# Kernel optimization log

Hardware: AMD Instinct MI355X
Metric: run time of the kernel (lower is better)

Reference implementation:

```python
import jax, jax.numpy as jnp
import numpy as np
from jax import lax

B, T, I, H = 64, 784, 1, 600


def setup_inputs() -> dict:
    key = jax.random.key(0)
    ks = jax.random.split(key, 9)
    k = 1.0 / np.sqrt(H)  # pytorch LSTMCell/Linear init scale
    x = jax.random.normal(ks[0], (B, T, I), dtype=jnp.float32)
    hs0 = jax.random.normal(ks[1], (B, H), dtype=jnp.float32)
    cs0 = jax.random.normal(ks[2], (B, H), dtype=jnp.float32)
    W_ih = jax.random.normal(ks[3], (4 * H, I), dtype=jnp.float32) * k
    W_hh = jax.random.normal(ks[4], (4 * H, H), dtype=jnp.float32) * k
    b_ih = jax.random.normal(ks[5], (4 * H,), dtype=jnp.float32) * k
    b_hh = jax.random.normal(ks[6], (4 * H,), dtype=jnp.float32) * k
    W_out = jax.random.normal(ks[7], (10, H), dtype=jnp.float32) * k
    b_out = jax.random.normal(ks[8], (10,), dtype=jnp.float32) * k
    return {"x": x, "hs0": hs0, "cs0": cs0, "W_ih": W_ih, "W_hh": W_hh,
            "b_ih": b_ih, "b_hh": b_hh, "W_out": W_out, "b_out": b_out}


def reference(x, hs0, cs0, W_ih, W_hh, b_ih, b_hh, W_out, b_out):
    # Precompute input projections for all timesteps in one GEMM: [B,T,4H]
    pre = jnp.einsum('bti,gi->btg', x, W_ih) + b_ih + b_hh
    pre_t = jnp.swapaxes(pre, 0, 1)  # [T,B,4H]

    def step(carry, p):
        h, c = carry
        gates = p + h @ W_hh.T  # [B,4H], pytorch gate order i,f,g,o
        i, f, g, o = jnp.split(gates, 4, axis=-1)
        c = jax.nn.sigmoid(f) * c + jax.nn.sigmoid(i) * jnp.tanh(g)
        h = jax.nn.sigmoid(o) * jnp.tanh(c)
        return (h, c), None

    (h, _), _ = lax.scan(step, (hs0, cs0), pre_t)
    return h @ W_out.T + b_out  # [B,10]
```

## Files before the change

### kernel.cpp

```cpp
#include <hip/hip_runtime.h>
#include <math.h>

#define BB 64
#define TT 784
#define HH 600
#define CG 50
#define SGN 4
#define CPW 12
#define BW 16
#define NWG (CG*SGN)
#define BLOCK 512
#define HB4 (BW*150)
#define LDS_BYTES (84*1024)

typedef float f2v __attribute__((ext_vector_type(2)));

__device__ __forceinline__ void ldg5_bypass(const float4* g0, const float4* g1,
                                            const float4* g2, const float4* g3,
                                            const float4* g4,
                                            float4& a, float4& b, float4& c,
                                            float4& d, float4& e) {
    asm volatile(
        "global_load_dwordx4 %0, %5, off sc0 sc1\n\t"
        "global_load_dwordx4 %1, %6, off sc0 sc1\n\t"
        "global_load_dwordx4 %2, %7, off sc0 sc1\n\t"
        "global_load_dwordx4 %3, %8, off sc0 sc1\n\t"
        "global_load_dwordx4 %4, %9, off sc0 sc1\n\t"
        "s_waitcnt vmcnt(0)"
        : "=&v"(a), "=&v"(b), "=&v"(c), "=&v"(d), "=&v"(e)
        : "v"(g0), "v"(g1), "v"(g2), "v"(g3), "v"(g4)
        : "memory");
}

__device__ __forceinline__ void ldg6_slice(const float4* base,
                                           float4& a, float4& b, float4& c,
                                           float4& d, float4& e, float4& f) {
    asm volatile(
        "global_load_dwordx4 %0, %6, off sc0 sc1\n\t"
        "global_load_dwordx4 %1, %6, off offset:16 sc0 sc1\n\t"
        "global_load_dwordx4 %2, %6, off offset:32 sc0 sc1\n\t"
        "global_load_dwordx4 %3, %6, off offset:2400 sc0 sc1\n\t"
        "global_load_dwordx4 %4, %6, off offset:2416 sc0 sc1\n\t"
        "global_load_dwordx4 %5, %6, off offset:2432 sc0 sc1\n\t"
        "s_waitcnt vmcnt(0)"
        : "=&v"(a), "=&v"(b), "=&v"(c), "=&v"(d), "=&v"(e), "=&v"(f)
        : "v"(base) : "memory");
}

__device__ __forceinline__ void stg_bypass(float* p, float v) {
    asm volatile("global_store_dword %0, %1, off sc0 sc1"
                 :: "v"(p), "v"(v) : "memory");
}

__device__ __forceinline__ float sigm_f(float v) {
    return 1.f / (1.f + __expf(-v));
}
__device__ __forceinline__ float tanh_f(float v) {
    return 1.f - 2.f / (__expf(2.f * v) + 1.f);
}

template<int MASK, int CNT>
__device__ __forceinline__ void fold(float* v, int kh) {
    const bool hi = (kh & MASK) != 0;
    #pragma unroll
    for (int i = 0; i < CNT; ++i) {
        float send = hi ? v[i] : v[i + CNT];
        float recv = __shfl_xor(send, MASK);
        v[i] = (hi ? v[i + CNT] : v[i]) + recv;
    }
}

extern "C" __global__ void __launch_bounds__(BLOCK, 2)
lstm_main(const float* __restrict__ x, const float* __restrict__ hs0,
          const float* __restrict__ cs0, const float* __restrict__ W_ih,
          const float* __restrict__ W_hh, const float* __restrict__ b_ih,
          const float* __restrict__ b_hh, float* __restrict__ hbuf,
          unsigned int* __restrict__ flags)
{
    extern __shared__ float lds[];
    float4* h4l  = (float4*)lds;
    float*  g_lds = lds + 4 * HB4;

    const int wg   = blockIdx.x;
    const int cg   = wg % CG;
    const int sg   = wg / CG;
    const int tid  = threadIdx.x;
    const int w    = tid >> 6;
    const int lane = tid & 63;
    const int bh   = lane >> 5;
    const int kh   = lane & 31;
    const int khc  = (kh < 30) ? kh : 29;
    const int b0   = sg * BW;

    f2v Wr2[6][10];
    #pragma unroll
    for (int r = 0; r < 6; ++r) {
        const int row = 6 * w + r;
        const int g   = row / 12, c = row % 12;
        const float* wrow = W_hh + ((size_t)g * HH + cg * CPW + c) * HH + khc * 20;
        #pragma unroll
        for (int j = 0; j < 5; ++j) {
            float4 t4 = (kh < 30) ? *(const float4*)(wrow + 4 * j)
                                  : make_float4(0.f, 0.f, 0.f, 0.f);
            Wr2[r][2 * j]     = (f2v){t4.x, t4.y};
            Wr2[r][2 * j + 1] = (f2v){t4.z, t4.w};
        }
    }

    float wihv[4], biasv[4], cst = 0.f;
    const int pc = tid >> 4, pb = tid & 15;
    const int cell = cg * CPW + pc;
    const int bglob = b0 + pb;
    if (tid < 192) {
        #pragma unroll
        for (int g = 0; g < 4; ++g) {
            const int grow = g * HH + cell;
            wihv[g]  = W_ih[grow];
            biasv[g] = b_ih[grow] + b_hh[grow];
        }
        cst = cs0[(size_t)bglob * HH + cell];
    }

    const int i0 = tid, i1 = tid + 512, i2 = tid + 1024, i3 = tid + 1536;
    const int i4 = (tid + 2048 < HB4) ? tid + 2048 : HB4 - 1;

    const int sp    = tid >> 3;
    const int bsl   = tid & 7;
    const unsigned int* pflag = &flags[(sg * CG + sp) * 16];
    const int pdst  = (2 * bsl) * 150 + 3 * sp;

    unsigned int* myflag = &flags[wg * 16];

    for (int t = 0; t < TT; ++t) {
        float xv = 0.f;
        if (tid < 192) xv = x[(size_t)bglob * TT + t];

        if (t == 0) {
            const float4* s4 = (const float4*)hs0 + (size_t)b0 * 150;
            float4 v0, v1, v2, v3, v4;
            ldg5_bypass(s4 + i0, s4 + i1, s4 + i2, s4 + i3, s4 + i4,
                        v0, v1, v2, v3, v4);
            h4l[i0] = v0; h4l[i1] = v1; h4l[i2] = v2; h4l[i3] = v3; h4l[i4] = v4;
        } else if (tid < 400) {
            while (__hip_atomic_load(pflag, __ATOMIC_RELAXED,
                                     __HIP_MEMORY_SCOPE_AGENT) < (unsigned)t)
                __builtin_amdgcn_s_sleep(1);
            const float4* src = (const float4*)(hbuf + (size_t)(t & 1) * BB * HH
                + (size_t)(b0 + 2 * bsl) * HH + CPW * sp);
            float4 r0, r1, r2, r3, r4, r5;
            ldg6_slice(src, r0, r1, r2, r3, r4, r5);
            h4l[pdst]       = r0; h4l[pdst + 1]       = r1; h4l[pdst + 2]       = r2;
            h4l[pdst + 150] = r3; h4l[pdst + 150 + 1] = r4; h4l[pdst + 150 + 2] = r5;
        }
        __syncthreads();

        float v[48];
        {
            f2v acc2[6][8];
            #pragma unroll
            for (int r = 0; r < 6; ++r)
                #pragma unroll
                for (int bi = 0; bi < 8; ++bi)
                    acc2[r][bi] = (f2v){0.f, 0.f};

            const float4* hb_base = h4l + (size_t)bh * 8 * 150 + khc * 5;
            #pragma unroll
            for (int bi = 0; bi < 8; ++bi) {
                const float4* hb = hb_base + bi * 150;
                const float4 A = hb[0], B = hb[1], C = hb[2],
                             D = hb[3], E = hb[4];
                f2v h2[10];
                h2[0] = (f2v){A.x, A.y}; h2[1] = (f2v){A.z, A.w};
                h2[2] = (f2v){B.x, B.y}; h2[3] = (f2v){B.z, B.w};
                h2[4] = (f2v){C.x, C.y}; h2[5] = (f2v){C.z, C.w};
                h2[6] = (f2v){D.x, D.y}; h2[7] = (f2v){D.z, D.w};
                h2[8] = (f2v){E.x, E.y}; h2[9] = (f2v){E.z, E.w};
                #pragma unroll
                for (int r = 0; r < 6; ++r)
                    #pragma unroll
                    for (int j = 0; j < 10; ++j)
                        acc2[r][bi] = __builtin_elementwise_fma(Wr2[r][j],
                                                                h2[j],
                                                                acc2[r][bi]);
            }
            #pragma unroll
            for (int r = 0; r < 6; ++r)
                #pragma unroll
                for (int bi = 0; bi < 8; ++bi)
                    v[r * 8 + bi] = acc2[r][bi][0] + acc2[r][bi][1];
        }

        fold<16, 24>(v, kh);
        fold<8, 12>(v, kh);
        fold<4, 6>(v, kh);
        fold<2, 3>(v, kh);
        #pragma unroll
        for (int i = 0; i < 3; ++i)
            v[i] += __shfl_xor(v[i], 1);

        if (!(kh & 1)) {
            const int vb = 3 * (kh >> 1);
            #pragma unroll
            for (int s = 0; s < 3; ++s) {
                const int val = vb + s;
                const int rowl = val >> 3, bi = val & 7;
                g_lds[(6 * w + rowl) * 16 + bh * 8 + bi] = v[s];
            }
        }
        __syncthreads();

        float* hdst = hbuf + (size_t)((t + 1) & 1) * BB * HH;
        if (tid < 192) {
            const float gi = g_lds[(0 * 12 + pc) * 16 + pb] + xv * wihv[0] + biasv[0];
            const float gf = g_lds[(1 * 12 + pc) * 16 + pb] + xv * wihv[1] + biasv[1];
            const float gg = g_lds[(2 * 12 + pc) * 16 + pb] + xv * wihv[2] + biasv[2];
            const float go = g_lds[(3 * 12 + pc) * 16 + pb] + xv * wihv[3] + biasv[3];
            const float cn = sigm_f(gf) * cst + sigm_f(gi) * tanh_f(gg);
            cst = cn;
            stg_bypass(&hdst[(size_t)bglob * HH + cell], sigm_f(go) * tanh_f(cn));
        }
        asm volatile("s_waitcnt vmcnt(0)" ::: "memory");
        __syncthreads();
        if (tid == 0)
            __hip_atomic_store(myflag, (unsigned)(t + 1), __ATOMIC_RELAXED,
                               __HIP_MEMORY_SCOPE_AGENT);
    }
}

extern "C" __global__ void lstm_out(const float* __restrict__ hbuf0,
                                    const float* __restrict__ W_out,
                                    const float* __restrict__ b_out,
                                    float* __restrict__ out)
{
    int b = blockIdx.x;
    int lane = threadIdx.x;
    float acc[10] = {};
    for (int k = lane; k < HH; k += 64) {
        float hv = hbuf0[(size_t)b * HH + k];
        #pragma unroll
        for (int o = 0; o < 10; ++o)
            acc[o] += hv * W_out[(size_t)o * HH + k];
    }
    #pragma unroll
    for (int o = 0; o < 10; ++o) {
        float v = acc[o];
        for (int off = 32; off > 0; off >>= 1) v += __shfl_down(v, off);
        if (lane == 0) out[b * 10 + o] = v + b_out[o];
    }
}

extern "C" void kernel_launch(void* const* d_in, const int* in_sizes, int n_in,
                              void* d_out, int out_size, void* d_ws, size_t ws_size,
                              hipStream_t stream)
{
    const float* x     = (const float*)d_in[0];
    const float* hs0   = (const float*)d_in[1];
    const float* cs0   = (const float*)d_in[2];
    const float* W_ih  = (const float*)d_in[3];
    const float* W_hh  = (const float*)d_in[4];
    const float* b_ih  = (const float*)d_in[5];
    const float* b_hh  = (const float*)d_in[6];
    const float* W_out = (const float*)d_in[7];
    const float* b_out = (const float*)d_in[8];
    float* out = (float*)d_out;

    float* hbuf = (float*)d_ws;
    unsigned int* flags = (unsigned int*)((char*)d_ws + (size_t)2 * BB * HH * sizeof(float));

    hipFuncSetAttribute((const void*)lstm_main,
                        hipFuncAttributeMaxDynamicSharedMemorySize, LDS_BYTES);

    hipMemsetAsync(flags, 0, NWG * 16 * sizeof(unsigned int), stream);
    hipLaunchKernelGGL(lstm_main, dim3(NWG), dim3(BLOCK), LDS_BYTES, stream,
                       x, hs0, cs0, W_ih, W_hh, b_ih, b_hh, hbuf, flags);
    hipLaunchKernelGGL(lstm_out, dim3(BB), dim3(64), 0, stream,
                       hbuf, W_out, b_out, out);
}
```

Before: 5.119 ms.

## Poll all producer flags first, then bulk-load the h slice with all threads

Previously, 400 threads each polled the flag of one producer group and loaded that group's 12-cell slice of h. Now 50 threads poll all the flags, a block barrier follows, and all 512 threads read the block's full 16x600 h tile with wide bypass loads. The same code path also covers the t==0 load from hs0. This spreads the copy evenly across threads, but it makes every block wait for the slowest producer before any loading starts and adds a second __syncthreads per step. The h-vector unpacking is also switched to a reinterpret cast, which is cosmetic.

```diff
diff --git a/kernel.cpp b/kernel.cpp
--- a/kernel.cpp
+++ b/kernel.cpp
@@ -32,21 +32,6 @@
         : "memory");
 }
 
-__device__ __forceinline__ void ldg6_slice(const float4* base,
-                                           float4& a, float4& b, float4& c,
-                                           float4& d, float4& e, float4& f) {
-    asm volatile(
-        "global_load_dwordx4 %0, %6, off sc0 sc1\n\t"
-        "global_load_dwordx4 %1, %6, off offset:16 sc0 sc1\n\t"
-        "global_load_dwordx4 %2, %6, off offset:32 sc0 sc1\n\t"
-        "global_load_dwordx4 %3, %6, off offset:2400 sc0 sc1\n\t"
-        "global_load_dwordx4 %4, %6, off offset:2416 sc0 sc1\n\t"
-        "global_load_dwordx4 %5, %6, off offset:2432 sc0 sc1\n\t"
-        "s_waitcnt vmcnt(0)"
-        : "=&v"(a), "=&v"(b), "=&v"(c), "=&v"(d), "=&v"(e), "=&v"(f)
-        : "v"(base) : "memory");
-}
-
 __device__ __forceinline__ void stg_bypass(float* p, float v) {
     asm volatile("global_store_dword %0, %1, off sc0 sc1"
                  :: "v"(p), "v"(v) : "memory");
@@ -124,33 +109,29 @@
     const int i0 = tid, i1 = tid + 512, i2 = tid + 1024, i3 = tid + 1536;
     const int i4 = (tid + 2048 < HB4) ? tid + 2048 : HB4 - 1;
 
-    const int sp    = tid >> 3;
-    const int bsl   = tid & 7;
-    const unsigned int* pflag = &flags[(sg * CG + sp) * 16];
-    const int pdst  = (2 * bsl) * 150 + 3 * sp;
-
     unsigned int* myflag = &flags[wg * 16];
 
     for (int t = 0; t < TT; ++t) {
         float xv = 0.f;
         if (tid < 192) xv = x[(size_t)bglob * TT + t];
 
-        if (t == 0) {
-            const float4* s4 = (const float4*)hs0 + (size_t)b0 * 150;
+        if (t > 0) {
+            if (tid < CG) {
+                const unsigned int* f = &flags[(sg * CG + tid) * 16];
+                while (__hip_atomic_load(f, __ATOMIC_RELAXED,
+                                         __HIP_MEMORY_SCOPE_AGENT) < (unsigned)t)
+                    __builtin_amdgcn_s_sleep(1);
+            }
+        }
+        __syncthreads();
+
+        {
+            const float* hsrc = (t == 0) ? hs0 : (hbuf + (size_t)(t & 1) * BB * HH);
+            const float4* s4 = (const float4*)hsrc + (size_t)b0 * 150;
             float4 v0, v1, v2, v3, v4;
             ldg5_bypass(s4 + i0, s4 + i1, s4 + i2, s4 + i3, s4 + i4,
                         v0, v1, v2, v3, v4);
             h4l[i0] = v0; h4l[i1] = v1; h4l[i2] = v2; h4l[i3] = v3; h4l[i4] = v4;
-        } else if (tid < 400) {
-            while (__hip_atomic_load(pflag, __ATOMIC_RELAXED,
-                                     __HIP_MEMORY_SCOPE_AGENT) < (unsigned)t)
-                __builtin_amdgcn_s_sleep(1);
-            const float4* src = (const float4*)(hbuf + (size_t)(t & 1) * BB * HH
-                + (size_t)(b0 + 2 * bsl) * HH + CPW * sp);
-            float4 r0, r1, r2, r3, r4, r5;
-            ldg6_slice(src, r0, r1, r2, r3, r4, r5);
-            h4l[pdst]       = r0; h4l[pdst + 1]       = r1; h4l[pdst + 2]       = r2;
-            h4l[pdst + 150] = r3; h4l[pdst + 150 + 1] = r4; h4l[pdst + 150 + 2] = r5;
         }
         __syncthreads();
 
@@ -167,14 +148,10 @@
             #pragma unroll
             for (int bi = 0; bi < 8; ++bi) {
                 const float4* hb = hb_base + bi * 150;
-                const float4 A = hb[0], B = hb[1], C = hb[2],
-                             D = hb[3], E = hb[4];
-                f2v h2[10];
-                h2[0] = (f2v){A.x, A.y}; h2[1] = (f2v){A.z, A.w};
-                h2[2] = (f2v){B.x, B.y}; h2[3] = (f2v){B.z, B.w};
-                h2[4] = (f2v){C.x, C.y}; h2[5] = (f2v){C.z, C.w};
-                h2[6] = (f2v){D.x, D.y}; h2[7] = (f2v){D.z, D.w};
-                h2[8] = (f2v){E.x, E.y}; h2[9] = (f2v){E.z, E.w};
+                float4 hv[5];
+                hv[0] = hb[0]; hv[1] = hb[1]; hv[2] = hb[2];
+                hv[3] = hb[3]; hv[4] = hb[4];
+                const f2v* h2 = (const f2v*)hv;
                 #pragma unroll
                 for (int r = 0; r < 6; ++r)
                     #pragma unroll
```

New measurement: 4.499 ms. 1.14x faster.
